# Kernel tuning notes

Hardware: AMD Instinct MI355X
Metric: run time of the kernel (lower is better)

The kernel has to match this reference:

```python
import jax, jax.numpy as jnp
import numpy as np

B, IN, H, OUT = 256, 512, 1024, 512
S, Wd, SH = 512, 256, 3          # memory_slots, memory_width, shift_range
P_READ = Wd + 2 + SH + 1         # key, beta, gate, shift(3), gamma
P_WRITE = P_READ + 2 * Wd        # + erase, add


def setup_inputs() -> dict:
    key = jax.random.key(0)
    ks = jax.random.split(key, 8)
    sc = 0.02
    return {
        "x": jax.random.normal(ks[0], (B, IN), jnp.float32),
        "W_ih": jax.random.normal(ks[1], (4 * H, IN + Wd), jnp.float32) * sc,
        "b_ih": jnp.zeros((4 * H,), jnp.float32),
        "W_hh": jax.random.normal(ks[2], (4 * H, H), jnp.float32) * sc,
        "b_hh": jnp.zeros((4 * H,), jnp.float32),
        "W_read": jax.random.normal(ks[3], (P_READ, H), jnp.float32) * sc,
        "b_read": jnp.zeros((P_READ,), jnp.float32),
        "W_write": jax.random.normal(ks[4], (P_WRITE, H), jnp.float32) * sc,
        "b_write": jnp.zeros((P_WRITE,), jnp.float32),
        "W_out": jax.random.normal(ks[5], (OUT, H + Wd), jnp.float32) * sc,
        "b_out": jnp.zeros((OUT,), jnp.float32),
        "mem_bias": jax.random.normal(ks[6], (S, Wd), jnp.float32) * sc,
    }


def _content_address(key_v, beta, memory):
    # cosine similarity of key [B,Wd] vs memory [B,S,Wd], eps=1e-8 like torch
    num = jnp.einsum('bw,bsw->bs', key_v, memory)
    kn = jnp.maximum(jnp.linalg.norm(key_v, axis=1, keepdims=True), 1e-8)
    mn = jnp.maximum(jnp.linalg.norm(memory, axis=2), 1e-8)
    sim = num / (kn * mn) * beta[:, None]
    return jax.nn.softmax(sim, axis=1)


def _address(p, prev_w, memory):
    # content_and_location addressing for a single head
    key_v = p[:, :Wd]
    beta = jax.nn.softplus(p[:, Wd])
    gate = jax.nn.sigmoid(p[:, Wd + 1])
    shift = jax.nn.softmax(p[:, Wd + 2:Wd + 2 + SH], axis=1)
    gamma = 1.0 + jax.nn.softplus(p[:, Wd + 2 + SH])
    cw = _content_address(key_v, beta, memory)
    g = gate[:, None]
    gw = g * cw + (1.0 - g) * prev_w  # interpolation gate
    # circular shift: shifted[pos] = s0*w[pos-1] + s1*w[pos] + s2*w[pos+1]
    sw = (shift[:, 0:1] * jnp.roll(gw, 1, axis=1)
          + shift[:, 1:2] * gw
          + shift[:, 2:3] * jnp.roll(gw, -1, axis=1))
    sp = sw ** gamma[:, None]  # sharpening
    return sp / (jnp.sum(sp, axis=1, keepdims=True) + 1e-6)


def reference(x, W_ih, b_ih, W_hh, b_hh, W_read, b_read, W_write, b_write, W_out, b_out, mem_bias):
    Bb = x.shape[0]
    # init_state (prev_state=None path)
    memory = jnp.broadcast_to(mem_bias[None], (Bb, S, Wd))
    w0 = jnp.zeros((Bb, S), x.dtype).at[:, 0].set(1.0)
    rv = jnp.zeros((Bb, Wd), x.dtype)
    h = jnp.zeros((Bb, H), x.dtype)
    c = jnp.zeros((Bb, H), x.dtype)
    # LSTMCell controller
    inp = jnp.concatenate([x, rv], axis=1)
    gates = inp @ W_ih.T + b_ih + h @ W_hh.T + b_hh
    i, f, g, o = jnp.split(gates, 4, axis=1)
    c = jax.nn.sigmoid(f) * c + jax.nn.sigmoid(i) * jnp.tanh(g)
    h = jax.nn.sigmoid(o) * jnp.tanh(c)
    # read head addressing (1 head)
    rp = h @ W_read.T + b_read
    read_w = _address(rp, w0, memory)
    # write head addressing + erase/add (1 head)
    wp = h @ W_write.T + b_write
    write_w = _address(wp, w0, memory)
    erase = jax.nn.sigmoid(wp[:, P_READ:P_READ + Wd])
    add = jnp.tanh(wp[:, P_READ + Wd:])
    memory = memory * (1.0 - write_w[:, :, None] * erase[:, None, :]) + write_w[:, :, None] * add[:, None, :]
    # read after write
    rv = jnp.einsum('bsw,bs->bw', memory, read_w)
    out = jnp.concatenate([h, rv], axis=1) @ W_out.T + b_out
    return out
```

## Files before the change

### kernel.cpp

```cpp
#include <hip/hip_runtime.h>
#include <hip/hip_bf16.h>
#include <math.h>

#define BB   256
#define INW  512
#define HH   1024
#define OUTW 512
#define SS   512
#define WD   256
#define P_READ  262
#define P_WRITE 774
#define RW_LD   1056
#define W_OFF   272

typedef __attribute__((ext_vector_type(8))) short bf16x8;
typedef __attribute__((ext_vector_type(4))) float f32x4;

__device__ __forceinline__ float sigmoidf(float x) { return 1.f / (1.f + expf(-x)); }
__device__ __forceinline__ float softplusf(float x) { return (x > 20.f) ? x : log1pf(expf(x)); }
__device__ __forceinline__ unsigned short f2b(float f) {
    union { float f; unsigned u; } c; c.f = f;
    return (unsigned short)((c.u + 0x7FFFu + ((c.u >> 16) & 1u)) >> 16);
}
__device__ __forceinline__ void st_bf4(__hip_bfloat16* d, float a, float b, float c, float e) {
    ushort4 u; u.x = f2b(a); u.y = f2b(b); u.z = f2b(c); u.w = f2b(e);
    *reinterpret_cast<ushort4*>(d) = u;
}
__device__ __forceinline__ float wave_sum(float v) {
    #pragma unroll
    for (int off = 32; off > 0; off >>= 1) v += __shfl_down(v, off, 64);
    return v;
}

#define N_WIH (3072*512)
#define N_WRW (RW_LD*1024)
#define N_WO  (512*1280)
#define N_X   (256*512)
#define N_MB  (512*256)
#define N_MT  (256*512)
#define N_BIA 3072
#define N_BRW RW_LD
#define N_TOT (N_WIH+N_WRW+N_WO+N_X+N_MB+N_MT+N_BIA+N_BRW)
#define NB_CVT ((N_TOT/4 + 255) / 256)

__global__ __launch_bounds__(256)
void convert_all(const float* __restrict__ W_ih, const float* __restrict__ b_ih,
                 const float* __restrict__ b_hh,
                 const float* __restrict__ W_read, const float* __restrict__ b_read,
                 const float* __restrict__ W_write, const float* __restrict__ b_write,
                 const float* __restrict__ W_out, const float* __restrict__ x,
                 const float* __restrict__ mem,
                 __hip_bfloat16* __restrict__ Wih_c, __hip_bfloat16* __restrict__ Wrw_p,
                 __hip_bfloat16* __restrict__ Wo_b, __hip_bfloat16* __restrict__ x_b,
                 __hip_bfloat16* __restrict__ mem_b, __hip_bfloat16* __restrict__ memT_b,
                 float* __restrict__ bias_c, float* __restrict__ bias_rw,
                 float* __restrict__ mem_norm)
{
    if (blockIdx.x >= NB_CVT) {
        __shared__ float red[4];
        int s = blockIdx.x - NB_CVT;
        float v = mem[(size_t)s * WD + threadIdx.x];
        float vv = wave_sum(v * v);
        if ((threadIdx.x & 63) == 0) red[threadIdx.x >> 6] = vv;
        __syncthreads();
        if (threadIdx.x == 0)
            mem_norm[s] = fmaxf(sqrtf(red[0] + red[1] + red[2] + red[3]), 1e-8f);
        return;
    }
    long i = ((long)blockIdx.x * 256 + threadIdx.x) * 4;
    if (i >= N_TOT) return;
    if (i < N_WIH) {
        int r = (int)(i >> 9), c = (int)(i & 511);
        int sr = r < 1024 ? r : r + 1024;
        float4 v = *reinterpret_cast<const float4*>(W_ih + (size_t)sr * 768 + c);
        st_bf4(Wih_c + i, v.x, v.y, v.z, v.w);
        return;
    }
    i -= N_WIH;
    if (i < N_WRW) {
        int r = (int)(i >> 10), c = (int)(i & 1023);
        float4 v = make_float4(0.f, 0.f, 0.f, 0.f);
        if (r < W_OFF) { if (r < P_READ) v = *reinterpret_cast<const float4*>(W_read + (size_t)r * 1024 + c); }
        else { int wr = r - W_OFF; if (wr < P_WRITE) v = *reinterpret_cast<const float4*>(W_write + (size_t)wr * 1024 + c); }
        st_bf4(Wrw_p + i, v.x, v.y, v.z, v.w);
        return;
    }
    i -= N_WRW;
    if (i < N_WO) {
        float4 v = *reinterpret_cast<const float4*>(W_out + i);
        st_bf4(Wo_b + i, v.x, v.y, v.z, v.w);
        return;
    }
    i -= N_WO;
    if (i < N_X) {
        float4 v = *reinterpret_cast<const float4*>(x + i);
        st_bf4(x_b + i, v.x, v.y, v.z, v.w);
        return;
    }
    i -= N_X;
    if (i < N_MB) {
        float4 v = *reinterpret_cast<const float4*>(mem + i);
        st_bf4(mem_b + i, v.x, v.y, v.z, v.w);
        return;
    }
    i -= N_MB;
    if (i < N_MT) {
        int w = (int)(i >> 9), s = (int)(i & 511);
        st_bf4(memT_b + i, mem[(size_t)s * 256 + w], mem[(size_t)(s + 1) * 256 + w],
               mem[(size_t)(s + 2) * 256 + w], mem[(size_t)(s + 3) * 256 + w]);
        return;
    }
    i -= N_MT;
    if (i < N_BIA) {
        #pragma unroll
        for (int u = 0; u < 4; ++u) {
            long r = i + u;
            long sr = r < 1024 ? r : r + 1024;
            bias_c[r] = b_ih[sr] + b_hh[sr];
        }
        return;
    }
    i -= N_BIA;
    {
        #pragma unroll
        for (int u = 0; u < 4; ++u) {
            long r = i + u;
            float v = 0.f;
            if (r < W_OFF) { if (r < P_READ) v = b_read[r]; }
            else { long wr = r - W_OFF; if (wr < P_WRITE) v = b_write[wr]; }
            bias_rw[r] = v;
        }
    }
}

__global__ __launch_bounds__(64)
void gemm_gates(const __hip_bfloat16* __restrict__ x_b,
                const __hip_bfloat16* __restrict__ Wih_c,
                const float* __restrict__ bias_c,
                __hip_bfloat16* __restrict__ h_b)
{
    const int l = threadIdx.x;
    const int bn = blockIdx.x * 16;
    const int bm = blockIdx.y * 16;
    const int r = l & 15, q = l >> 4;
    const __hip_bfloat16* ap = x_b + (size_t)(bm + r) * INW + q * 8;
    const __hip_bfloat16* bi = Wih_c + (size_t)(bn + r) * INW + q * 8;
    const __hip_bfloat16* bg = bi + (size_t)1024 * INW;
    const __hip_bfloat16* bo = bi + (size_t)2048 * INW;
    f32x4 ai = {0.f,0.f,0.f,0.f}, ag = ai, ao = ai;
    #pragma unroll
    for (int k = 0; k < INW; k += 32) {
        bf16x8 a = *reinterpret_cast<const bf16x8*>(ap + k);
        ai = __builtin_amdgcn_mfma_f32_16x16x32_bf16(a, *reinterpret_cast<const bf16x8*>(bi + k), ai, 0, 0, 0);
        ag = __builtin_amdgcn_mfma_f32_16x16x32_bf16(a, *reinterpret_cast<const bf16x8*>(bg + k), ag, 0, 0, 0);
        ao = __builtin_amdgcn_mfma_f32_16x16x32_bf16(a, *reinterpret_cast<const bf16x8*>(bo + k), ao, 0, 0, 0);
    }
    const int j = bn + r;
    const float bii = bias_c[j], big = bias_c[1024 + j], bio = bias_c[2048 + j];
    #pragma unroll
    for (int jj = 0; jj < 4; ++jj) {
        int b = bm + q * 4 + jj;
        float c = sigmoidf(ai[jj] + bii) * tanhf(ag[jj] + big);
        h_b[(size_t)b * HH + j] = __float2bfloat16(sigmoidf(ao[jj] + bio) * tanhf(c));
    }
}

__global__ __launch_bounds__(64)
void gemm_dual(const __hip_bfloat16* __restrict__ h_b,
               const __hip_bfloat16* __restrict__ Wrw_p,
               const __hip_bfloat16* __restrict__ Wo_b,
               const float* __restrict__ bias_rw, const float* __restrict__ b_out,
               float* __restrict__ rpwp, float* __restrict__ out,
               __hip_bfloat16* __restrict__ keys)
{
    const int bid = blockIdx.x;
    const int lane = threadIdx.x;
    const int r = lane & 15, q = lane >> 4;
    int bm, bn, ldb;
    const __hip_bfloat16* B;
    if (bid < 1056) { int nt = bid % 66, mt = bid / 66; bm = mt * 16; bn = nt * 16; B = Wrw_p; ldb = HH; }
    else { int o = bid - 1056; int nt = o & 31, mt = o >> 5; bm = mt * 16; bn = nt * 16; B = Wo_b; ldb = 1280; }

    const __hip_bfloat16* ap = h_b + (size_t)(bm + r) * HH + q * 8;
    const __hip_bfloat16* bp = B + (size_t)(bn + r) * ldb + q * 8;
    f32x4 a0 = {0.f,0.f,0.f,0.f}, a1 = a0;
    #pragma unroll 8
    for (int k = 0; k < 512; k += 32) {
        a0 = __builtin_amdgcn_mfma_f32_16x16x32_bf16(
            *reinterpret_cast<const bf16x8*>(ap + k),
            *reinterpret_cast<const bf16x8*>(bp + k), a0, 0, 0, 0);
        a1 = __builtin_amdgcn_mfma_f32_16x16x32_bf16(
            *reinterpret_cast<const bf16x8*>(ap + 512 + k),
            *reinterpret_cast<const bf16x8*>(bp + 512 + k), a1, 0, 0, 0);
    }
    const int col = bn + r;
    if (bid < 1056) {
        const float bv = bias_rw[col];
        #pragma unroll
        for (int j = 0; j < 4; ++j) {
            int m = bm + q * 4 + j;
            float v = a0[j] + a1[j] + bv;
            rpwp[(size_t)m * RW_LD + col] = v;
            if (col < WD)
                keys[(size_t)m * WD + col] = __float2bfloat16(v);
            else if (col >= W_OFF && col < W_OFF + WD)
                keys[(size_t)(256 + m) * WD + (col - W_OFF)] = __float2bfloat16(v);
        }
    } else {
        const float bv = b_out[col];
        #pragma unroll
        for (int j = 0; j < 4; ++j) {
            int m = bm + q * 4 + j;
            out[(size_t)m * OUTW + col] = a0[j] + a1[j] + bv;
        }
    }
}

__global__ __launch_bounds__(64)
void gemm_num(const __hip_bfloat16* __restrict__ keys,
              const __hip_bfloat16* __restrict__ mem_b,
              const float* __restrict__ mem_norm,
              float* __restrict__ numd)
{
    const int l = threadIdx.x;
    const int bn = blockIdx.x * 16;
    const int bm = blockIdx.y * 16;
    const int r = l & 15, q = l >> 4;
    const __hip_bfloat16* ap = keys + (size_t)(bm + r) * WD + q * 8;
    const __hip_bfloat16* bp = mem_b + (size_t)(bn + r) * WD + q * 8;
    f32x4 acc = {0.f,0.f,0.f,0.f};
    #pragma unroll
    for (int k = 0; k < WD; k += 32)
        acc = __builtin_amdgcn_mfma_f32_16x16x32_bf16(
            *reinterpret_cast<const bf16x8*>(ap + k),
            *reinterpret_cast<const bf16x8*>(bp + k), acc, 0, 0, 0);
    const int col = bn + r;
    const float inv = 1.f / mem_norm[col];
    #pragma unroll
    for (int j = 0; j < 4; ++j)
        numd[(size_t)(bm + q * 4 + j) * SS + col] = acc[j] * inv;
}

__device__ __forceinline__ void redpair_sum(float& a, float& b, volatile float* redA, volatile float* redB) {
    #pragma unroll
    for (int off = 32; off > 0; off >>= 1) { a += __shfl_down(a, off, 64); b += __shfl_down(b, off, 64); }
    int wid = threadIdx.x >> 6;
    __syncthreads();
    if ((threadIdx.x & 63) == 0) { redA[wid] = a; redB[wid] = b; }
    __syncthreads();
    a = redA[0]+redA[1]+redA[2]+redA[3]+redA[4]+redA[5]+redA[6]+redA[7];
    b = redB[0]+redB[1]+redB[2]+redB[3]+redB[4]+redB[5]+redB[6]+redB[7];
}
__device__ __forceinline__ void redpair_max(float& a, float& b, volatile float* redA, volatile float* redB) {
    #pragma unroll
    for (int off = 32; off > 0; off >>= 1) { a = fmaxf(a, __shfl_down(a, off, 64)); b = fmaxf(b, __shfl_down(b, off, 64)); }
    int wid = threadIdx.x >> 6;
    __syncthreads();
    if ((threadIdx.x & 63) == 0) { redA[wid] = a; redB[wid] = b; }
    __syncthreads();
    a = fmaxf(fmaxf(fmaxf(redA[0],redA[1]),fmaxf(redA[2],redA[3])),fmaxf(fmaxf(redA[4],redA[5]),fmaxf(redA[6],redA[7])));
    b = fmaxf(fmaxf(fmaxf(redB[0],redB[1]),fmaxf(redB[2],redB[3])),fmaxf(fmaxf(redB[4],redB[5]),fmaxf(redB[6],redB[7])));
}

__global__ __launch_bounds__(512)
void address_fused(const float* __restrict__ rpwp, const float* __restrict__ numd,
                   __hip_bfloat16* __restrict__ A12, float* __restrict__ t3)
{
    const int b = blockIdx.x;
    const int t = threadIdx.x;
    const float* pr = rpwp + (size_t)b * RW_LD;
    const float* pw = pr + W_OFF;

    __shared__ float redA[8], redB[8];
    __shared__ float bufr[SS], bufw[SS];

    float beta_r  = softplusf(pr[WD]);
    float gate_r  = sigmoidf(pr[WD + 1]);
    float r0 = pr[WD+2], r1 = pr[WD+3], r2 = pr[WD+4];
    float rmx = fmaxf(r0, fmaxf(r1, r2));
    float re0 = expf(r0-rmx), re1 = expf(r1-rmx), re2 = expf(r2-rmx);
    float rinv = 1.f / (re0+re1+re2);
    float shr0 = re0*rinv, shr1 = re1*rinv, shr2 = re2*rinv;
    float gamma_r = 1.f + softplusf(pr[WD + 5]);

    float beta_w  = softplusf(pw[WD]);
    float gate_w  = sigmoidf(pw[WD + 1]);
    float w0 = pw[WD+2], w1 = pw[WD+3], w2 = pw[WD+4];
    float wmx = fmaxf(w0, fmaxf(w1, w2));
    float we0 = expf(w0-wmx), we1 = expf(w1-wmx), we2 = expf(w2-wmx);
    float winv = 1.f / (we0+we1+we2);
    float shw0 = we0*winv, shw1 = we1*winv, shw2 = we2*winv;
    float gamma_w = 1.f + softplusf(pw[WD + 5]);

    {
        float kv = (t < WD) ? pr[t] : pw[t - WD];
        float vv = kv * kv;
        #pragma unroll
        for (int off = 32; off > 0; off >>= 1) vv += __shfl_down(vv, off, 64);
        int wid = t >> 6;
        if ((t & 63) == 0) redA[wid] = vv;
        __syncthreads();
    }
    float knr = fmaxf(sqrtf(redA[0]+redA[1]+redA[2]+redA[3]), 1e-8f);
    float knw = fmaxf(sqrtf(redA[4]+redA[5]+redA[6]+redA[7]), 1e-8f);
    __syncthreads();

    float sim_r = numd[(size_t)b * SS + t]         / knr * beta_r;
    float sim_w = numd[(size_t)(256 + b) * SS + t] / knw * beta_w;

    float mr = sim_r, mw = sim_w;
    redpair_max(mr, mw, redA, redB);
    float exr = expf(sim_r - mr), exw = expf(sim_w - mw);
    float sr = exr, sw = exw;
    redpair_sum(sr, sw, redA, redB);
    float cwr = exr / sr, cww = exw / sw;

    float onehot = (t == 0) ? 1.f : 0.f;
    float gwr = gate_r * cwr + (1.f - gate_r) * onehot;
    float gww = gate_w * cww + (1.f - gate_w) * onehot;
    __syncthreads();
    bufr[t] = gwr; bufw[t] = gww;
    __syncthreads();

    int tm = (t + SS - 1) & (SS - 1), tp = (t + 1) & (SS - 1);
    float swr = shr0 * bufr[tm] + shr1 * gwr + shr2 * bufr[tp];
    float sww = shw0 * bufw[tm] + shw1 * gww + shw2 * bufw[tp];

    float spr = powf(fmaxf(swr, 0.f), gamma_r), spw = powf(fmaxf(sww, 0.f), gamma_w);
    float ssr = spr, ssw = spw;
    redpair_sum(ssr, ssw, redA, redB);
    float rfin = spr / (ssr + 1e-6f);
    float wfin = spw / (ssw + 1e-6f);

    float prod = rfin * wfin;
    A12[(size_t)b * SS + t] = __float2bfloat16(rfin);
    A12[(size_t)(256 + b) * SS + t] = __float2bfloat16(prod);
    float tp3 = prod, dummy = 0.f;
    redpair_sum(tp3, dummy, redA, redB);
    if (t == 0) t3[b] = tp3;
}

__global__ __launch_bounds__(64)
void gemm_t12rv(const __hip_bfloat16* __restrict__ A12,
                const __hip_bfloat16* __restrict__ memT_b,
                const float* __restrict__ rpwp, const float* __restrict__ t3,
                __hip_bfloat16* __restrict__ rv_b)
{
    const int l = threadIdx.x;
    const int bn = blockIdx.x * 16;
    const int bm = blockIdx.y * 16;
    const int r = l & 15, q = l >> 4;
    const __hip_bfloat16* a1 = A12 + (size_t)(bm + r) * SS + q * 8;
    const __hip_bfloat16* a2 = a1 + (size_t)256 * SS;
    const __hip_bfloat16* bp = memT_b + (size_t)(bn + r) * SS + q * 8;
    f32x4 acc1 = {0.f,0.f,0.f,0.f}, acc2 = acc1;
    #pragma unroll
    for (int k = 0; k < SS; k += 32) {
        bf16x8 bb = *reinterpret_cast<const bf16x8*>(bp + k);
        acc1 = __builtin_amdgcn_mfma_f32_16x16x32_bf16(*reinterpret_cast<const bf16x8*>(a1 + k), bb, acc1, 0, 0, 0);
        acc2 = __builtin_amdgcn_mfma_f32_16x16x32_bf16(*reinterpret_cast<const bf16x8*>(a2 + k), bb, acc2, 0, 0, 0);
    }
    const int w = bn + r;
    #pragma unroll
    for (int j = 0; j < 4; ++j) {
        int b = bm + q * 4 + j;
        const float* row = rpwp + (size_t)b * RW_LD;
        float e = sigmoidf(row[W_OFF + P_READ + w]);
        float a = tanhf(row[W_OFF + P_READ + WD + w]);
        float rv = acc1[j] - e * acc2[j] + a * t3[b];
        rv_b[(size_t)b * WD + w] = __float2bfloat16(rv);
    }
}

__global__ __launch_bounds__(64)
void gemm_outrv(const __hip_bfloat16* __restrict__ rv_b,
                const __hip_bfloat16* __restrict__ Wo_b,
                float* __restrict__ out)
{
    const int l = threadIdx.x;
    const int bn = blockIdx.x * 16;
    const int bm = blockIdx.y * 16;
    const int r = l & 15, q = l >> 4;
    const __hip_bfloat16* ap = rv_b + (size_t)(bm + r) * WD + q * 8;
    const __hip_bfloat16* bp = Wo_b + (size_t)(bn + r) * 1280 + 1024 + q * 8;
    f32x4 acc = {0.f,0.f,0.f,0.f};
    #pragma unroll
    for (int k = 0; k < WD; k += 32)
        acc = __builtin_amdgcn_mfma_f32_16x16x32_bf16(
            *reinterpret_cast<const bf16x8*>(ap + k),
            *reinterpret_cast<const bf16x8*>(bp + k), acc, 0, 0, 0);
    const int col = bn + r;
    #pragma unroll
    for (int j = 0; j < 4; ++j) {
        int m = bm + q * 4 + j;
        out[(size_t)m * OUTW + col] += acc[j];
    }
}

extern "C" void kernel_launch(void* const* d_in, const int* in_sizes, int n_in,
                              void* d_out, int out_size, void* d_ws, size_t ws_size,
                              hipStream_t stream)
{
    const float* x       = (const float*)d_in[0];
    const float* W_ih    = (const float*)d_in[1];
    const float* b_ih    = (const float*)d_in[2];
    const float* b_hh    = (const float*)d_in[4];
    const float* W_read  = (const float*)d_in[5];
    const float* b_read  = (const float*)d_in[6];
    const float* W_write = (const float*)d_in[7];
    const float* b_write = (const float*)d_in[8];
    const float* W_out   = (const float*)d_in[9];
    const float* b_out   = (const float*)d_in[10];
    const float* mem     = (const float*)d_in[11];

    float* ws = (float*)d_ws;
    float* rpwp     = ws;
    float* numd     = ws + 270336;
    float* bias_c   = ws + 532480;
    float* bias_rw  = ws + 535552;
    float* mem_norm = ws + 536608;
    float* t3       = ws + 537120;
    __hip_bfloat16* bfb = (__hip_bfloat16*)(ws + 537376);
    __hip_bfloat16* x_b    = bfb;
    __hip_bfloat16* Wih_c  = bfb + 131072;
    __hip_bfloat16* Wrw_p  = bfb + 1703936;
    __hip_bfloat16* Wo_b   = bfb + 2785280;
    __hip_bfloat16* mem_b  = bfb + 3440640;
    __hip_bfloat16* memT_b = bfb + 3571712;
    __hip_bfloat16* h_b    = bfb + 3702784;
    __hip_bfloat16* keys   = bfb + 3964928;
    __hip_bfloat16* A12    = bfb + 4096000;
    __hip_bfloat16* rv_b   = bfb + 4358144;
    float* out = (float*)d_out;

    convert_all<<<NB_CVT + SS, 256, 0, stream>>>(
        W_ih, b_ih, b_hh, W_read, b_read, W_write, b_write, W_out, x, mem,
        Wih_c, Wrw_p, Wo_b, x_b, mem_b, memT_b, bias_c, bias_rw, mem_norm);
    gemm_gates<<<dim3(64, 16), 64, 0, stream>>>(x_b, Wih_c, bias_c, h_b);
    gemm_dual<<<1568, 64, 0, stream>>>(h_b, Wrw_p, Wo_b, bias_rw, b_out, rpwp, out, keys);
    gemm_num<<<dim3(32, 32), 64, 0, stream>>>(keys, mem_b, mem_norm, numd);
    address_fused<<<BB, 512, 0, stream>>>(rpwp, numd, A12, t3);
    gemm_t12rv<<<dim3(16, 16), 64, 0, stream>>>(A12, memT_b, rpwp, t3, rv_b);
    gemm_outrv<<<dim3(32, 16), 64, 0, stream>>>(rv_b, Wo_b, out);
}
```

Baseline: 59.03 us.

## Fuse fp32-to-bf16 conversion into GEMM operand loads, drop convert_all pre-pass

Removes the separate conversion kernel that cast every weight, input and memory tensor to bf16 and packed biases. Each GEMM now reads the fp32 operands directly and rounds them to bf16 in registers. Memory norms are computed inside k_num, and the memory transpose moves into extra blocks of the gates kernel. This saves one launch and the write-then-reread round trip through the workspace. In exchange, fp32 loads are twice as wide and repeated conversion work is done across tiles that share the same B operand.

After: 79.45 us. +34.6%, slower.

```diff
diff --git a/kernel.cpp b/kernel.cpp
--- a/kernel.cpp
+++ b/kernel.cpp
@@ -22,141 +22,51 @@
     union { float f; unsigned u; } c; c.f = f;
     return (unsigned short)((c.u + 0x7FFFu + ((c.u >> 16) & 1u)) >> 16);
 }
-__device__ __forceinline__ void st_bf4(__hip_bfloat16* d, float a, float b, float c, float e) {
-    ushort4 u; u.x = f2b(a); u.y = f2b(b); u.z = f2b(c); u.w = f2b(e);
-    *reinterpret_cast<ushort4*>(d) = u;
-}
-__device__ __forceinline__ float wave_sum(float v) {
-    #pragma unroll
-    for (int off = 32; off > 0; off >>= 1) v += __shfl_down(v, off, 64);
-    return v;
-}
-
-#define N_WIH (3072*512)
-#define N_WRW (RW_LD*1024)
-#define N_WO  (512*1280)
-#define N_X   (256*512)
-#define N_MB  (512*256)
-#define N_MT  (256*512)
-#define N_BIA 3072
-#define N_BRW RW_LD
-#define N_TOT (N_WIH+N_WRW+N_WO+N_X+N_MB+N_MT+N_BIA+N_BRW)
-#define NB_CVT ((N_TOT/4 + 255) / 256)
-
-__global__ __launch_bounds__(256)
-void convert_all(const float* __restrict__ W_ih, const float* __restrict__ b_ih,
-                 const float* __restrict__ b_hh,
-                 const float* __restrict__ W_read, const float* __restrict__ b_read,
-                 const float* __restrict__ W_write, const float* __restrict__ b_write,
-                 const float* __restrict__ W_out, const float* __restrict__ x,
-                 const float* __restrict__ mem,
-                 __hip_bfloat16* __restrict__ Wih_c, __hip_bfloat16* __restrict__ Wrw_p,
-                 __hip_bfloat16* __restrict__ Wo_b, __hip_bfloat16* __restrict__ x_b,
-                 __hip_bfloat16* __restrict__ mem_b, __hip_bfloat16* __restrict__ memT_b,
-                 float* __restrict__ bias_c, float* __restrict__ bias_rw,
-                 float* __restrict__ mem_norm)
-{
-    if (blockIdx.x >= NB_CVT) {
-        __shared__ float red[4];
-        int s = blockIdx.x - NB_CVT;
-        float v = mem[(size_t)s * WD + threadIdx.x];
-        float vv = wave_sum(v * v);
-        if ((threadIdx.x & 63) == 0) red[threadIdx.x >> 6] = vv;
-        __syncthreads();
-        if (threadIdx.x == 0)
-            mem_norm[s] = fmaxf(sqrtf(red[0] + red[1] + red[2] + red[3]), 1e-8f);
+__device__ __forceinline__ bf16x8 cvt8(const float* p) {
+    float4 lo = *reinterpret_cast<const float4*>(p);
+    float4 hi = *reinterpret_cast<const float4*>(p + 4);
+    bf16x8 r;
+    r[0] = (short)f2b(lo.x); r[1] = (short)f2b(lo.y); r[2] = (short)f2b(lo.z); r[3] = (short)f2b(lo.w);
+    r[4] = (short)f2b(hi.x); r[5] = (short)f2b(hi.y); r[6] = (short)f2b(hi.z); r[7] = (short)f2b(hi.w);
+    return r;
+}
+
+__global__ __launch_bounds__(64)
+void k_gates(const float* __restrict__ x, const float* __restrict__ W_ih,
+             const float* __restrict__ b_ih, const float* __restrict__ b_hh,
+             const float* __restrict__ mem,
+             __hip_bfloat16* __restrict__ h_b, __hip_bfloat16* __restrict__ memT_b)
+{
+    const int bid = blockIdx.x;
+    const int lane = threadIdx.x;
+    if (bid >= 1024) {
+        int wb = (bid - 1024) * 4;
+        for (int i = 0; i < 4; ++i) {
+            int wr = wb + i;
+            for (int s = lane; s < SS; s += 64)
+                memT_b[(size_t)wr * SS + s] = __float2bfloat16(mem[(size_t)s * WD + wr]);
+        }
         return;
     }
-    long i = ((long)blockIdx.x * 256 + threadIdx.x) * 4;
-    if (i >= N_TOT) return;
-    if (i < N_WIH) {
-        int r = (int)(i >> 9), c = (int)(i & 511);
-        int sr = r < 1024 ? r : r + 1024;
-        float4 v = *reinterpret_cast<const float4*>(W_ih + (size_t)sr * 768 + c);
-        st_bf4(Wih_c + i, v.x, v.y, v.z, v.w);
-        return;
-    }
-    i -= N_WIH;
-    if (i < N_WRW) {
-        int r = (int)(i >> 10), c = (int)(i & 1023);
-        float4 v = make_float4(0.f, 0.f, 0.f, 0.f);
-        if (r < W_OFF) { if (r < P_READ) v = *reinterpret_cast<const float4*>(W_read + (size_t)r * 1024 + c); }
-        else { int wr = r - W_OFF; if (wr < P_WRITE) v = *reinterpret_cast<const float4*>(W_write + (size_t)wr * 1024 + c); }
-        st_bf4(Wrw_p + i, v.x, v.y, v.z, v.w);
-        return;
-    }
-    i -= N_WRW;
-    if (i < N_WO) {
-        float4 v = *reinterpret_cast<const float4*>(W_out + i);
-        st_bf4(Wo_b + i, v.x, v.y, v.z, v.w);
-        return;
-    }
-    i -= N_WO;
-    if (i < N_X) {
-        float4 v = *reinterpret_cast<const float4*>(x + i);
-        st_bf4(x_b + i, v.x, v.y, v.z, v.w);
-        return;
-    }
-    i -= N_X;
-    if (i < N_MB) {
-        float4 v = *reinterpret_cast<const float4*>(mem + i);
-        st_bf4(mem_b + i, v.x, v.y, v.z, v.w);
-        return;
-    }
-    i -= N_MB;
-    if (i < N_MT) {
-        int w = (int)(i >> 9), s = (int)(i & 511);
-        st_bf4(memT_b + i, mem[(size_t)s * 256 + w], mem[(size_t)(s + 1) * 256 + w],
-               mem[(size_t)(s + 2) * 256 + w], mem[(size_t)(s + 3) * 256 + w]);
-        return;
-    }
-    i -= N_MT;
-    if (i < N_BIA) {
-        #pragma unroll
-        for (int u = 0; u < 4; ++u) {
-            long r = i + u;
-            long sr = r < 1024 ? r : r + 1024;
-            bias_c[r] = b_ih[sr] + b_hh[sr];
-        }
-        return;
-    }
-    i -= N_BIA;
-    {
-        #pragma unroll
-        for (int u = 0; u < 4; ++u) {
-            long r = i + u;
-            float v = 0.f;
-            if (r < W_OFF) { if (r < P_READ) v = b_read[r]; }
-            else { long wr = r - W_OFF; if (wr < P_WRITE) v = b_write[wr]; }
-            bias_rw[r] = v;
-        }
-    }
-}
-
-__global__ __launch_bounds__(64)
-void gemm_gates(const __hip_bfloat16* __restrict__ x_b,
-                const __hip_bfloat16* __restrict__ Wih_c,
-                const float* __restrict__ bias_c,
-                __hip_bfloat16* __restrict__ h_b)
-{
-    const int l = threadIdx.x;
-    const int bn = blockIdx.x * 16;
-    const int bm = blockIdx.y * 16;
-    const int r = l & 15, q = l >> 4;
-    const __hip_bfloat16* ap = x_b + (size_t)(bm + r) * INW + q * 8;
-    const __hip_bfloat16* bi = Wih_c + (size_t)(bn + r) * INW + q * 8;
-    const __hip_bfloat16* bg = bi + (size_t)1024 * INW;
-    const __hip_bfloat16* bo = bi + (size_t)2048 * INW;
+    const int bn = (bid & 63) * 16;
+    const int bm = (bid >> 6) * 16;
+    const int r = lane & 15, q = lane >> 4;
+    const float* axp = x    + (size_t)(bm + r) * INW + q * 8;
+    const float* bip = W_ih + (size_t)(bn + r) * 768 + q * 8;
+    const float* bgp = W_ih + (size_t)(2048 + bn + r) * 768 + q * 8;
+    const float* bop = W_ih + (size_t)(3072 + bn + r) * 768 + q * 8;
     f32x4 ai = {0.f,0.f,0.f,0.f}, ag = ai, ao = ai;
     #pragma unroll
     for (int k = 0; k < INW; k += 32) {
-        bf16x8 a = *reinterpret_cast<const bf16x8*>(ap + k);
-        ai = __builtin_amdgcn_mfma_f32_16x16x32_bf16(a, *reinterpret_cast<const bf16x8*>(bi + k), ai, 0, 0, 0);
-        ag = __builtin_amdgcn_mfma_f32_16x16x32_bf16(a, *reinterpret_cast<const bf16x8*>(bg + k), ag, 0, 0, 0);
-        ao = __builtin_amdgcn_mfma_f32_16x16x32_bf16(a, *reinterpret_cast<const bf16x8*>(bo + k), ao, 0, 0, 0);
+        bf16x8 a = cvt8(axp + k);
+        ai = __builtin_amdgcn_mfma_f32_16x16x32_bf16(a, cvt8(bip + k), ai, 0, 0, 0);
+        ag = __builtin_amdgcn_mfma_f32_16x16x32_bf16(a, cvt8(bgp + k), ag, 0, 0, 0);
+        ao = __builtin_amdgcn_mfma_f32_16x16x32_bf16(a, cvt8(bop + k), ao, 0, 0, 0);
     }
     const int j = bn + r;
-    const float bii = bias_c[j], big = bias_c[1024 + j], bio = bias_c[2048 + j];
+    const float bii = b_ih[j] + b_hh[j];
+    const float big = b_ih[2048 + j] + b_hh[2048 + j];
+    const float bio = b_ih[3072 + j] + b_hh[3072 + j];
     #pragma unroll
     for (int jj = 0; jj < 4; ++jj) {
         int b = bm + q * 4 + jj;
@@ -166,36 +76,43 @@
 }
 
 __global__ __launch_bounds__(64)
-void gemm_dual(const __hip_bfloat16* __restrict__ h_b,
-               const __hip_bfloat16* __restrict__ Wrw_p,
-               const __hip_bfloat16* __restrict__ Wo_b,
-               const float* __restrict__ bias_rw, const float* __restrict__ b_out,
-               float* __restrict__ rpwp, float* __restrict__ out,
-               __hip_bfloat16* __restrict__ keys)
+void k_dual(const __hip_bfloat16* __restrict__ h_b,
+            const float* __restrict__ W_read, const float* __restrict__ b_read,
+            const float* __restrict__ W_write, const float* __restrict__ b_write,
+            const float* __restrict__ W_out, const float* __restrict__ b_out,
+            float* __restrict__ rpwp, float* __restrict__ out,
+            __hip_bfloat16* __restrict__ keys)
 {
     const int bid = blockIdx.x;
     const int lane = threadIdx.x;
     const int r = lane & 15, q = lane >> 4;
-    int bm, bn, ldb;
-    const __hip_bfloat16* B;
-    if (bid < 1056) { int nt = bid % 66, mt = bid / 66; bm = mt * 16; bn = nt * 16; B = Wrw_p; ldb = HH; }
-    else { int o = bid - 1056; int nt = o & 31, mt = o >> 5; bm = mt * 16; bn = nt * 16; B = Wo_b; ldb = 1280; }
-
-    const __hip_bfloat16* ap = h_b + (size_t)(bm + r) * HH + q * 8;
-    const __hip_bfloat16* bp = B + (size_t)(bn + r) * ldb + q * 8;
-    f32x4 a0 = {0.f,0.f,0.f,0.f}, a1 = a0;
-    #pragma unroll 8
-    for (int k = 0; k < 512; k += 32) {
-        a0 = __builtin_amdgcn_mfma_f32_16x16x32_bf16(
-            *reinterpret_cast<const bf16x8*>(ap + k),
-            *reinterpret_cast<const bf16x8*>(bp + k), a0, 0, 0, 0);
-        a1 = __builtin_amdgcn_mfma_f32_16x16x32_bf16(
-            *reinterpret_cast<const bf16x8*>(ap + 512 + k),
-            *reinterpret_cast<const bf16x8*>(bp + 512 + k), a1, 0, 0, 0);
-    }
-    const int col = bn + r;
+    const bf16x8 z8 = {0,0,0,0,0,0,0,0};
+
     if (bid < 1056) {
-        const float bv = bias_rw[col];
+        const int nt = bid % 66, mt = bid / 66;
+        const int bm = mt * 16, bn = nt * 16;
+        const int brow = bn + r;
+        bool valid = true;
+        const float* bsrc;
+        if (brow < W_OFF) { valid = (brow < P_READ); bsrc = W_read + (size_t)(valid ? brow : 0) * 1024; }
+        else { int wr2 = brow - W_OFF; valid = (wr2 < P_WRITE); bsrc = W_write + (size_t)(valid ? wr2 : 0) * 1024; }
+        bsrc += q * 8;
+        const __hip_bfloat16* ap = h_b + (size_t)(bm + r) * HH + q * 8;
+        f32x4 a0 = {0.f,0.f,0.f,0.f}, a1 = a0;
+        #pragma unroll 8
+        for (int k = 0; k < 512; k += 32) {
+            bf16x8 b0 = cvt8(bsrc + k);
+            bf16x8 b1 = cvt8(bsrc + 512 + k);
+            if (!valid) { b0 = z8; b1 = z8; }
+            a0 = __builtin_amdgcn_mfma_f32_16x16x32_bf16(
+                *reinterpret_cast<const bf16x8*>(ap + k), b0, a0, 0, 0, 0);
+            a1 = __builtin_amdgcn_mfma_f32_16x16x32_bf16(
+                *reinterpret_cast<const bf16x8*>(ap + 512 + k), b1, a1, 0, 0, 0);
+        }
+        const int col = bn + r;
+        float bv = 0.f;
+        if (col < W_OFF) { if (col < P_READ) bv = b_read[col]; }
+        else { int wc = col - W_OFF; if (wc < P_WRITE) bv = b_write[wc]; }
         #pragma unroll
         for (int j = 0; j < 4; ++j) {
             int m = bm + q * 4 + j;
@@ -207,6 +124,20 @@
                 keys[(size_t)(256 + m) * WD + (col - W_OFF)] = __float2bfloat16(v);
         }
     } else {
+        const int o = bid - 1056;
+        const int nt = o & 31, mt = o >> 5;
+        const int bm = mt * 16, bn = nt * 16;
+        const __hip_bfloat16* ap = h_b + (size_t)(bm + r) * HH + q * 8;
+        const float* bp = W_out + (size_t)(bn + r) * 1280 + q * 8;
+        f32x4 a0 = {0.f,0.f,0.f,0.f}, a1 = a0;
+        #pragma unroll 8
+        for (int k = 0; k < 512; k += 32) {
+            a0 = __builtin_amdgcn_mfma_f32_16x16x32_bf16(
+                *reinterpret_cast<const bf16x8*>(ap + k), cvt8(bp + k), a0, 0, 0, 0);
+            a1 = __builtin_amdgcn_mfma_f32_16x16x32_bf16(
+                *reinterpret_cast<const bf16x8*>(ap + 512 + k), cvt8(bp + 512 + k), a1, 0, 0, 0);
+        }
+        const int col = bn + r;
         const float bv = b_out[col];
         #pragma unroll
         for (int j = 0; j < 4; ++j) {
@@ -217,25 +148,33 @@
 }
 
 __global__ __launch_bounds__(64)
-void gemm_num(const __hip_bfloat16* __restrict__ keys,
-              const __hip_bfloat16* __restrict__ mem_b,
-              const float* __restrict__ mem_norm,
-              float* __restrict__ numd)
-{
-    const int l = threadIdx.x;
+void k_num(const __hip_bfloat16* __restrict__ keys, const float* __restrict__ mem,
+           float* __restrict__ numd)
+{
+    const int lane = threadIdx.x;
     const int bn = blockIdx.x * 16;
     const int bm = blockIdx.y * 16;
-    const int r = l & 15, q = l >> 4;
+    const int r = lane & 15, q = lane >> 4;
     const __hip_bfloat16* ap = keys + (size_t)(bm + r) * WD + q * 8;
-    const __hip_bfloat16* bp = mem_b + (size_t)(bn + r) * WD + q * 8;
+    const float* bp = mem + (size_t)(bn + r) * WD + q * 8;
     f32x4 acc = {0.f,0.f,0.f,0.f};
-    #pragma unroll
-    for (int k = 0; k < WD; k += 32)
+    float nn = 0.f;
+    #pragma unroll
+    for (int k = 0; k < WD; k += 32) {
+        float4 lo = *reinterpret_cast<const float4*>(bp + k);
+        float4 hi = *reinterpret_cast<const float4*>(bp + k + 4);
+        nn += lo.x*lo.x + lo.y*lo.y + lo.z*lo.z + lo.w*lo.w
+            + hi.x*hi.x + hi.y*hi.y + hi.z*hi.z + hi.w*hi.w;
+        bf16x8 bf;
+        bf[0]=(short)f2b(lo.x); bf[1]=(short)f2b(lo.y); bf[2]=(short)f2b(lo.z); bf[3]=(short)f2b(lo.w);
+        bf[4]=(short)f2b(hi.x); bf[5]=(short)f2b(hi.y); bf[6]=(short)f2b(hi.z); bf[7]=(short)f2b(hi.w);
         acc = __builtin_amdgcn_mfma_f32_16x16x32_bf16(
-            *reinterpret_cast<const bf16x8*>(ap + k),
-            *reinterpret_cast<const bf16x8*>(bp + k), acc, 0, 0, 0);
+            *reinterpret_cast<const bf16x8*>(ap + k), bf, acc, 0, 0, 0);
+    }
+    nn += __shfl_xor(nn, 16, 64);
+    nn += __shfl_xor(nn, 32, 64);
+    const float inv = 1.f / fmaxf(sqrtf(nn), 1e-8f);
     const int col = bn + r;
-    const float inv = 1.f / mem_norm[col];
     #pragma unroll
     for (int j = 0; j < 4; ++j)
         numd[(size_t)(bm + q * 4 + j) * SS + col] = acc[j] * inv;
@@ -373,22 +312,21 @@
 }
 
 __global__ __launch_bounds__(64)
-void gemm_outrv(const __hip_bfloat16* __restrict__ rv_b,
-                const __hip_bfloat16* __restrict__ Wo_b,
-                float* __restrict__ out)
+void k_outrv(const __hip_bfloat16* __restrict__ rv_b,
+             const float* __restrict__ W_out,
+             float* __restrict__ out)
 {
     const int l = threadIdx.x;
     const int bn = blockIdx.x * 16;
     const int bm = blockIdx.y * 16;
     const int r = l & 15, q = l >> 4;
     const __hip_bfloat16* ap = rv_b + (size_t)(bm + r) * WD + q * 8;
-    const __hip_bfloat16* bp = Wo_b + (size_t)(bn + r) * 1280 + 1024 + q * 8;
+    const float* bp = W_out + (size_t)(bn + r) * 1280 + 1024 + q * 8;
     f32x4 acc = {0.f,0.f,0.f,0.f};
     #pragma unroll
     for (int k = 0; k < WD; k += 32)
         acc = __builtin_amdgcn_mfma_f32_16x16x32_bf16(
-            *reinterpret_cast<const bf16x8*>(ap + k),
-            *reinterpret_cast<const bf16x8*>(bp + k), acc, 0, 0, 0);
+            *reinterpret_cast<const bf16x8*>(ap + k), cvt8(bp + k), acc, 0, 0, 0);
     const int col = bn + r;
     #pragma unroll
     for (int j = 0; j < 4; ++j) {
@@ -414,32 +352,22 @@
     const float* mem     = (const float*)d_in[11];
 
     float* ws = (float*)d_ws;
-    float* rpwp     = ws;
-    float* numd     = ws + 270336;
-    float* bias_c   = ws + 532480;
-    float* bias_rw  = ws + 535552;
-    float* mem_norm = ws + 536608;
-    float* t3       = ws + 537120;
-    __hip_bfloat16* bfb = (__hip_bfloat16*)(ws + 537376);
-    __hip_bfloat16* x_b    = bfb;
-    __hip_bfloat16* Wih_c  = bfb + 131072;
-    __hip_bfloat16* Wrw_p  = bfb + 1703936;
-    __hip_bfloat16* Wo_b   = bfb + 2785280;
-    __hip_bfloat16* mem_b  = bfb + 3440640;
-    __hip_bfloat16* memT_b = bfb + 3571712;
-    __hip_bfloat16* h_b    = bfb + 3702784;
-    __hip_bfloat16* keys   = bfb + 3964928;
-    __hip_bfloat16* A12    = bfb + 4096000;
-    __hip_bfloat16* rv_b   = bfb + 4358144;
+    float* rpwp = ws;
+    float* numd = ws + 270336;
+    float* t3   = ws + 532480;
+    __hip_bfloat16* bfb = (__hip_bfloat16*)(ws + 532736);
+    __hip_bfloat16* memT_b = bfb;
+    __hip_bfloat16* h_b    = bfb + 131072;
+    __hip_bfloat16* keys   = bfb + 393216;
+    __hip_bfloat16* A12    = bfb + 524288;
+    __hip_bfloat16* rv_b   = bfb + 786432;
     float* out = (float*)d_out;
 
-    convert_all<<<NB_CVT + SS, 256, 0, stream>>>(
-        W_ih, b_ih, b_hh, W_read, b_read, W_write, b_write, W_out, x, mem,
-        Wih_c, Wrw_p, Wo_b, x_b, mem_b, memT_b, bias_c, bias_rw, mem_norm);
-    gemm_gates<<<dim3(64, 16), 64, 0, stream>>>(x_b, Wih_c, bias_c, h_b);
-    gemm_dual<<<1568, 64, 0, stream>>>(h_b, Wrw_p, Wo_b, bias_rw, b_out, rpwp, out, keys);
-    gemm_num<<<dim3(32, 32), 64, 0, stream>>>(keys, mem_b, mem_norm, numd);
+    k_gates<<<1088, 64, 0, stream>>>(x, W_ih, b_ih, b_hh, mem, h_b, memT_b);
+    k_dual<<<1568, 64, 0, stream>>>(h_b, W_read, b_read, W_write, b_write,
+                                    W_out, b_out, rpwp, out, keys);
+    k_num<<<dim3(32, 32), 64, 0, stream>>>(keys, mem, numd);
     address_fused<<<BB, 512, 0, stream>>>(rpwp, numd, A12, t3);
     gemm_t12rv<<<dim3(16, 16), 64, 0, stream>>>(A12, memT_b, rpwp, t3, rv_b);
-    gemm_outrv<<<dim3(32, 16), 64, 0, stream>>>(rv_b, Wo_b, out);
-}
+    k_outrv<<<dim3(32, 16), 64, 0, stream>>>(rv_b, W_out, out);
+}
```
